# Performance work log

Hardware: AMD Instinct MI355X
Metric: run time of the kernel (lower is better)

The kernel has to match this reference:

```python
import jax, jax.numpy as jnp
import numpy as np

N_NODES = 100000
N_EDGES = 600000
IN_DIM = 128
HID = 128


def setup_inputs() -> dict:
    key = jax.random.key(0)
    ks = jax.random.split(key, 9)
    x = jax.random.normal(ks[0], (N_NODES, IN_DIM), dtype=jnp.float32)
    edge_index = jax.random.randint(ks[1], (2, N_EDGES), 0, N_NODES, dtype=jnp.int64)
    s = 1.0 / np.sqrt(IN_DIM)
    # PyG SAGEConv: out = lin_l(mean_aggr(x_src)) + lin_r(x_root); lin_l carries the bias.
    W_l0 = jax.random.uniform(ks[2], (IN_DIM, HID), jnp.float32, -s, s)
    b_l0 = jnp.zeros((HID,), jnp.float32)
    W_r0 = jax.random.uniform(ks[3], (IN_DIM, HID), jnp.float32, -s, s)
    s2 = 1.0 / np.sqrt(HID)
    W_l1 = jax.random.uniform(ks[4], (HID, HID), jnp.float32, -s2, s2)
    b_l1 = jnp.zeros((HID,), jnp.float32)
    W_r1 = jax.random.uniform(ks[5], (HID, HID), jnp.float32, -s2, s2)
    return {"x": x, "edge_index": edge_index,
            "W_l0": W_l0, "b_l0": b_l0, "W_r0": W_r0,
            "W_l1": W_l1, "b_l1": b_l1, "W_r1": W_r1}


def _sage_mean_conv(h, src, dst, W_l, b_l, W_r):
    # gather source-node features per edge, scatter-mean into destinations
    msgs = h[src]                                              # [E, D]
    sums = jax.ops.segment_sum(msgs, dst, num_segments=N_NODES)  # [N, D]
    cnt = jax.ops.segment_sum(jnp.ones((src.shape[0],), h.dtype), dst,
                              num_segments=N_NODES)             # [N]
    mean = sums / jnp.maximum(cnt, 1.0)[:, None]
    return mean @ W_l + b_l + h @ W_r


def reference(x, edge_index, W_l0, b_l0, W_r0, W_l1, b_l1, W_r1):
    src, dst = edge_index[0], edge_index[1]
    h = _sage_mean_conv(x, src, dst, W_l0, b_l0, W_r0)
    h = jax.nn.relu(h)  # dropout is identity in eval mode
    h = _sage_mean_conv(h, src, dst, W_l1, b_l1, W_r1)
    h = jax.nn.relu(h)
    return h
```

## Files before the change

### kernel.cpp

```cpp
#include <hip/hip_runtime.h>

#define N_NODES 100000
#define N_EDGES 600000
#define DIM 128

typedef __attribute__((ext_vector_type(8))) short bf16x8;
typedef __attribute__((ext_vector_type(4))) float f32x4;

typedef __attribute__((address_space(1))) const unsigned int g_u32;
typedef __attribute__((address_space(3))) unsigned int l_u32;
__device__ __forceinline__ void stage16(const void* g, void* l) {
  __builtin_amdgcn_global_load_lds((g_u32*)g, (l_u32*)l, 16, 0, 0);
}

__device__ __forceinline__ unsigned short f32_to_bf16_rn(float f) {
  unsigned int u = __builtin_bit_cast(unsigned int, f);
  unsigned int r = (u + 0x7FFFu + ((u >> 16) & 1u)) >> 16;
  return (unsigned short)r;
}

__global__ __launch_bounds__(256) void prep_k(
    const float* __restrict__ Wl0, const float* __restrict__ Wr0,
    const float* __restrict__ Wl1, const float* __restrict__ Wr1,
    unsigned short* __restrict__ P0, unsigned short* __restrict__ P1,
    const float* __restrict__ x, unsigned short* __restrict__ xhi,
    int* __restrict__ deg) {
  const int gid = blockIdx.x * 256 + threadIdx.x;
  if (gid < N_NODES) deg[gid] = 0;
  if (gid < 65536) {
    const int layer = gid >> 15;
    const int idx = gid & 32767;
    const int j = idx & 7;
    const int l = (idx >> 3) & 63;
    const int nt = (idx >> 9) & 7;
    const int g = idx >> 12;
    const int k = ((g & 3) << 5) + ((l >> 4) << 3) + j;
    const int n = (nt << 4) + (l & 15);
    const float* W = layer ? ((g < 4) ? Wl1 : Wr1) : ((g < 4) ? Wl0 : Wr0);
    (layer ? P1 : P0)[idx] = f32_to_bf16_rn(W[k * 128 + n]);
  } else {
    const int i = gid - 65536;
    if (i < N_NODES * DIM / 4) {
      const float4 v = reinterpret_cast<const float4*>(x)[i];
      const float f[4] = {v.x, v.y, v.z, v.w};
      unsigned short h[4];
#pragma unroll
      for (int j = 0; j < 4; ++j) h[j] = f32_to_bf16_rn(f[j]);
      uint2 hp;
      hp.x = (unsigned)h[0] | ((unsigned)h[1] << 16);
      hp.y = (unsigned)h[2] | ((unsigned)h[3] << 16);
      reinterpret_cast<uint2*>(xhi)[i] = hp;
    }
  }
}

__global__ void hist_k(const int* __restrict__ dst, int* __restrict__ deg) {
  int e = blockIdx.x * blockDim.x + threadIdx.x;
  if (e < N_EDGES) atomicAdd(&deg[dst[e]], 1);
}

__global__ __launch_bounds__(1024) void scan1_k(const int* __restrict__ deg,
                                                int* __restrict__ incl,
                                                int* __restrict__ bsum) {
  __shared__ int wsum[16];
  const int t = threadIdx.x, lane = t & 63, w = t >> 6;
  const int gi = blockIdx.x * 1024 + t;
  int v = (gi < N_NODES) ? deg[gi] : 0;
  int s = v;
#pragma unroll
  for (int off = 1; off < 64; off <<= 1) {
    int u = __shfl_up(s, off);
    if (lane >= off) s += u;
  }
  if (lane == 63) wsum[w] = s;
  __syncthreads();
  if (t < 16) {
    int ws = wsum[t];
#pragma unroll
    for (int off = 1; off < 16; off <<= 1) {
      int u = __shfl_up(ws, off);
      if (t >= off) ws += u;
    }
    wsum[t] = ws;
  }
  __syncthreads();
  const int val = s + (w ? wsum[w - 1] : 0);
  if (gi < N_NODES) incl[gi] = val;
  if (t == 1023) bsum[blockIdx.x] = val;
}

__global__ __launch_bounds__(1024) void scan3_k(const int* __restrict__ deg,
                                                const int* __restrict__ incl,
                                                const int* __restrict__ bsum,
                                                int* __restrict__ rowptr,
                                                int* __restrict__ head) {
  __shared__ int spart[2];
  __shared__ int boff_s;
  const int t = threadIdx.x;
  if (t < 128) {
    int v = (t < blockIdx.x) ? bsum[t] : 0;
#pragma unroll
    for (int off = 1; off < 64; off <<= 1) v += __shfl_xor(v, off);
    if ((t & 63) == 0) spart[t >> 6] = v;
  }
  __syncthreads();
  if (t == 0) boff_s = spart[0] + spart[1];
  __syncthreads();
  const int gi = blockIdx.x * 1024 + t;
  if (gi < N_NODES) {
    const int e = incl[gi] - deg[gi] + boff_s;
    rowptr[gi] = e;
    head[gi] = e;
  }
  if (gi == 0) rowptr[N_NODES] = N_EDGES;
}

__global__ void fill_k(const int* __restrict__ src, const int* __restrict__ dst,
                       int* __restrict__ head, int* __restrict__ col) {
  int e = blockIdx.x * blockDim.x + threadIdx.x;
  if (e < N_EDGES) {
    int p = atomicAdd(&head[dst[e]], 1);
    col[p] = src[e];
  }
}

__global__ __launch_bounds__(256) void agg_k(
    const unsigned short* __restrict__ plane, const int* __restrict__ rowptr,
    const int* __restrict__ col, unsigned short* __restrict__ mhi) {
  const int t = threadIdx.x;
  const int node = blockIdx.x * 16 + (t >> 4);
  const int q = t & 15;
  const int beg = rowptr[node], end = rowptr[node + 1];
  const uint4* P = reinterpret_cast<const uint4*>(plane);
  float a[8] = {};

  auto accum = [&](uint4 v) {
    const unsigned int u[4] = {v.x, v.y, v.z, v.w};
#pragma unroll
    for (int w = 0; w < 4; ++w) {
      a[2 * w] += __builtin_bit_cast(float, u[w] << 16);
      a[2 * w + 1] += __builtin_bit_cast(float, u[w] & 0xFFFF0000u);
    }
  };

  for (int i = beg; i < end; i += 4) {
    const int i1 = min(i + 1, end - 1);
    const int i2 = min(i + 2, end - 1);
    const int i3 = min(i + 3, end - 1);
    const int c0 = col[i], c1 = col[i1], c2 = col[i2], c3 = col[i3];
    const uint4 v0 = P[(size_t)c0 * 16 + q];
    const uint4 v1 = P[(size_t)c1 * 16 + q];
    const uint4 v2 = P[(size_t)c2 * 16 + q];
    const uint4 v3 = P[(size_t)c3 * 16 + q];
    accum(v0);
    if (i + 1 < end) accum(v1);
    if (i + 2 < end) accum(v2);
    if (i + 3 < end) accum(v3);
  }

  const int d = end - beg;
  const float inv = 1.0f / (float)(d > 1 ? d : 1);
  unsigned int hw[4];
#pragma unroll
  for (int w = 0; w < 4; ++w) {
    const unsigned short h0 = f32_to_bf16_rn(a[2 * w] * inv);
    const unsigned short h1 = f32_to_bf16_rn(a[2 * w + 1] * inv);
    hw[w] = (unsigned)h0 | ((unsigned)h1 << 16);
  }
  uint4 ho = {hw[0], hw[1], hw[2], hw[3]};
  reinterpret_cast<uint4*>(mhi)[(size_t)node * 16 + q] = ho;
}

template <int OUTF32>
__global__ __launch_bounds__(256, 4) void gemm_k(
    const unsigned short* __restrict__ Mhi, const unsigned short* __restrict__ Hhi,
    const unsigned short* __restrict__ Bp, const float* __restrict__ bias,
    unsigned short* __restrict__ Ohi, float* __restrict__ Of) {
  __shared__ unsigned short Bl[4][4096];
  const int t = threadIdx.x;
  const int lane = t & 63;
  const int wid = t >> 6;
  const int rbase = blockIdx.x * 64 + wid * 16;
  const int lm = lane & 15, lk = lane >> 4;
  const size_t r0 = (size_t)min(rbase + lm, N_NODES - 1);

  f32x4 acc[8] = {};

  auto stageG = [&](int g, int nb) {
#pragma unroll
    for (int c = 0; c < 2; ++c) {
      const int e = (c * 256 + t) * 8;
      stage16(Bp + (size_t)g * 4096 + e, &Bl[nb][e]);
    }
  };
  auto loadA = [&](int g) {
    const unsigned short* P = (g < 4) ? Mhi : Hhi;
    const int ke = ((g & 3) << 5) + (lk << 3);
    return *reinterpret_cast<const bf16x8*>(P + r0 * DIM + ke);
  };

  stageG(0, 0);
  stageG(1, 1);
  bf16x8 ca0 = loadA(0), ca1 = loadA(1), na0, na1;
  __syncthreads();

#pragma unroll
  for (int pg = 0; pg < 4; ++pg) {
    const int b0 = (2 * pg) & 3, b1 = (2 * pg + 1) & 3;
    if (pg < 3) {
      stageG(2 * pg + 2, (b0 + 2) & 3);
      stageG(2 * pg + 3, (b1 + 2) & 3);
      na0 = loadA(2 * pg + 2);
      na1 = loadA(2 * pg + 3);
    }
#pragma unroll
    for (int nt = 0; nt < 8; ++nt) {
      const bf16x8 b =
          *reinterpret_cast<const bf16x8*>(&Bl[b0][(nt * 64 + lane) * 8]);
      acc[nt] = __builtin_amdgcn_mfma_f32_16x16x32_bf16(ca0, b, acc[nt], 0, 0, 0);
    }
#pragma unroll
    for (int nt = 0; nt < 8; ++nt) {
      const bf16x8 b =
          *reinterpret_cast<const bf16x8*>(&Bl[b1][(nt * 64 + lane) * 8]);
      acc[nt] = __builtin_amdgcn_mfma_f32_16x16x32_bf16(ca1, b, acc[nt], 0, 0, 0);
    }
    __syncthreads();
    ca0 = na0;
    ca1 = na1;
  }

#pragma unroll
  for (int nt = 0; nt < 8; ++nt) {
    const int cidx = nt * 16 + lm;
    const float bv = bias[cidx];
#pragma unroll
    for (int i = 0; i < 4; ++i) {
      const int r = rbase + lk * 4 + i;
      if (r < N_NODES) {
        float v = acc[nt][i] + bv;
        v = fmaxf(v, 0.0f);
        if (OUTF32) {
          Of[(size_t)r * DIM + cidx] = v;
        } else {
          Ohi[(size_t)r * DIM + cidx] = f32_to_bf16_rn(v);
        }
      }
    }
  }
}

extern "C" void kernel_launch(void* const* d_in, const int* in_sizes, int n_in,
                              void* d_out, int out_size, void* d_ws,
                              size_t ws_size, hipStream_t stream) {
  const float* x = (const float*)d_in[0];
  const int* ei = (const int*)d_in[1];
  const float* Wl0 = (const float*)d_in[2];
  const float* bl0 = (const float*)d_in[3];
  const float* Wr0 = (const float*)d_in[4];
  const float* Wl1 = (const float*)d_in[5];
  const float* bl1 = (const float*)d_in[6];
  const float* Wr1 = (const float*)d_in[7];
  float* out = (float*)d_out;
  const int* src = ei;
  const int* dst = ei + N_EDGES;

  char* p = (char*)d_ws;
  auto alloc = [&](size_t bytes) {
    char* q = p;
    p += (bytes + 255) & ~(size_t)255;
    return q;
  };
  int* deg = (int*)alloc((size_t)N_NODES * 4);
  int* rowptr = (int*)alloc((size_t)(N_NODES + 1) * 4);
  int* head = (int*)alloc((size_t)N_NODES * 4);
  int* col = (int*)alloc((size_t)N_EDGES * 4);
  int* bsum = (int*)alloc(128 * 4);
  unsigned short* Bp0 = (unsigned short*)alloc(32768 * 2);
  unsigned short* Bp1 = (unsigned short*)alloc(32768 * 2);
  unsigned short* xhi = (unsigned short*)alloc((size_t)N_NODES * DIM * 2);
  unsigned short* mhi = (unsigned short*)alloc((size_t)N_NODES * DIM * 2);
  unsigned short* h1hi = (unsigned short*)alloc((size_t)N_NODES * DIM * 2);

  const int nScanB = (N_NODES + 1023) / 1024;

  prep_k<<<(65536 + N_NODES * DIM / 4 + 255) / 256, 256, 0, stream>>>(
      Wl0, Wr0, Wl1, Wr1, Bp0, Bp1, x, xhi, deg);
  hist_k<<<(N_EDGES + 255) / 256, 256, 0, stream>>>(dst, deg);
  scan1_k<<<nScanB, 1024, 0, stream>>>(deg, head, bsum);
  scan3_k<<<nScanB, 1024, 0, stream>>>(deg, head, bsum, rowptr, head);
  fill_k<<<(N_EDGES + 255) / 256, 256, 0, stream>>>(src, dst, head, col);

  const int nBlocks = (N_NODES + 63) / 64;
  const int aggBlocks = N_NODES / 16;

  agg_k<<<aggBlocks, 256, 0, stream>>>(xhi, rowptr, col, mhi);
  gemm_k<0><<<nBlocks, 256, 0, stream>>>(mhi, xhi, Bp0, bl0, h1hi, nullptr);
  agg_k<<<aggBlocks, 256, 0, stream>>>(h1hi, rowptr, col, mhi);
  gemm_k<1><<<nBlocks, 256, 0, stream>>>(mhi, h1hi, Bp1, bl1, nullptr, out);
}
```

Before: 182.0 us.

## Split GEMM tile by output columns per wave and drop block barriers

Each wave now covers all 64 rows of the block and a 32-column slice, instead of 16 rows and all 128 columns. Each wave therefore stages and reads only its own B fragments, which removes the block-wide __syncthreads. The LDS buffer shrinks to double buffering, and pipelining is done with explicit vmcnt waits. The trade-off is that A rows are now loaded redundantly by all four waves, four times more global or L2 reads of A, in exchange for less B LDS traffic and no barriers.

```diff
diff --git a/kernel.cpp b/kernel.cpp
--- a/kernel.cpp
+++ b/kernel.cpp
@@ -176,74 +176,85 @@
     const unsigned short* __restrict__ Mhi, const unsigned short* __restrict__ Hhi,
     const unsigned short* __restrict__ Bp, const float* __restrict__ bias,
     unsigned short* __restrict__ Ohi, float* __restrict__ Of) {
-  __shared__ unsigned short Bl[4][4096];
+  __shared__ unsigned short Bl[2][4096];
   const int t = threadIdx.x;
   const int lane = t & 63;
   const int wid = t >> 6;
-  const int rbase = blockIdx.x * 64 + wid * 16;
+  const int rbase = blockIdx.x * 64;
   const int lm = lane & 15, lk = lane >> 4;
-  const size_t r0 = (size_t)min(rbase + lm, N_NODES - 1);
-
-  f32x4 acc[8] = {};
+  size_t r[4];
+#pragma unroll
+  for (int mt = 0; mt < 4; ++mt)
+    r[mt] = (size_t)min(rbase + mt * 16 + lm, N_NODES - 1);
+
+  f32x4 acc[4][2] = {};
 
   auto stageG = [&](int g, int nb) {
 #pragma unroll
-    for (int c = 0; c < 2; ++c) {
-      const int e = (c * 256 + t) * 8;
-      stage16(Bp + (size_t)g * 4096 + e, &Bl[nb][e]);
+    for (int s = 0; s < 2; ++s) {
+      const int nt = 2 * wid + s;
+      stage16(Bp + ((size_t)(g * 8 + nt) * 64 + lane) * 8,
+              &Bl[nb][(nt * 64 + lane) * 8]);
     }
   };
-  auto loadA = [&](int g) {
+  auto loadA = [&](int g, bf16x8* a) {
     const unsigned short* P = (g < 4) ? Mhi : Hhi;
     const int ke = ((g & 3) << 5) + (lk << 3);
-    return *reinterpret_cast<const bf16x8*>(P + r0 * DIM + ke);
+#pragma unroll
+    for (int mt = 0; mt < 4; ++mt)
+      a[mt] = *reinterpret_cast<const bf16x8*>(P + r[mt] * DIM + ke);
   };
 
+  bf16x8 ca[4], na[4];
   stageG(0, 0);
-  stageG(1, 1);
-  bf16x8 ca0 = loadA(0), ca1 = loadA(1), na0, na1;
-  __syncthreads();
-
-#pragma unroll
-  for (int pg = 0; pg < 4; ++pg) {
-    const int b0 = (2 * pg) & 3, b1 = (2 * pg + 1) & 3;
-    if (pg < 3) {
-      stageG(2 * pg + 2, (b0 + 2) & 3);
-      stageG(2 * pg + 3, (b1 + 2) & 3);
-      na0 = loadA(2 * pg + 2);
-      na1 = loadA(2 * pg + 3);
-    }
-#pragma unroll
-    for (int nt = 0; nt < 8; ++nt) {
+  loadA(0, ca);
+
+#pragma unroll
+  for (int g = 0; g < 8; ++g) {
+    const int buf = g & 1;
+    if (g < 7) {
+      stageG(g + 1, buf ^ 1);
+      loadA(g + 1, na);
+      __builtin_amdgcn_sched_barrier(0);
+      asm volatile("s_waitcnt vmcnt(6)" ::: "memory");
+      __builtin_amdgcn_sched_barrier(0);
+    } else {
+      __builtin_amdgcn_sched_barrier(0);
+      asm volatile("s_waitcnt vmcnt(0)" ::: "memory");
+      __builtin_amdgcn_sched_barrier(0);
+    }
+#pragma unroll
+    for (int s = 0; s < 2; ++s) {
+      const int nt = 2 * wid + s;
       const bf16x8 b =
-          *reinterpret_cast<const bf16x8*>(&Bl[b0][(nt * 64 + lane) * 8]);
-      acc[nt] = __builtin_amdgcn_mfma_f32_16x16x32_bf16(ca0, b, acc[nt], 0, 0, 0);
-    }
-#pragma unroll
-    for (int nt = 0; nt < 8; ++nt) {
-      const bf16x8 b =
-          *reinterpret_cast<const bf16x8*>(&Bl[b1][(nt * 64 + lane) * 8]);
-      acc[nt] = __builtin_amdgcn_mfma_f32_16x16x32_bf16(ca1, b, acc[nt], 0, 0, 0);
-    }
-    __syncthreads();
-    ca0 = na0;
-    ca1 = na1;
-  }
-
-#pragma unroll
-  for (int nt = 0; nt < 8; ++nt) {
-    const int cidx = nt * 16 + lm;
+          *reinterpret_cast<const bf16x8*>(&Bl[buf][(nt * 64 + lane) * 8]);
+#pragma unroll
+      for (int mt = 0; mt < 4; ++mt)
+        acc[mt][s] = __builtin_amdgcn_mfma_f32_16x16x32_bf16(ca[mt], b, acc[mt][s], 0, 0, 0);
+    }
+    if (g < 7) {
+#pragma unroll
+      for (int mt = 0; mt < 4; ++mt) ca[mt] = na[mt];
+    }
+  }
+
+#pragma unroll
+  for (int s = 0; s < 2; ++s) {
+    const int cidx = (2 * wid + s) * 16 + lm;
     const float bv = bias[cidx];
 #pragma unroll
-    for (int i = 0; i < 4; ++i) {
-      const int r = rbase + lk * 4 + i;
-      if (r < N_NODES) {
-        float v = acc[nt][i] + bv;
-        v = fmaxf(v, 0.0f);
-        if (OUTF32) {
-          Of[(size_t)r * DIM + cidx] = v;
-        } else {
-          Ohi[(size_t)r * DIM + cidx] = f32_to_bf16_rn(v);
+    for (int mt = 0; mt < 4; ++mt) {
+#pragma unroll
+      for (int i = 0; i < 4; ++i) {
+        const int rr = rbase + mt * 16 + lk * 4 + i;
+        if (rr < N_NODES) {
+          float v = acc[mt][s][i] + bv;
+          v = fmaxf(v, 0.0f);
+          if (OUTF32) {
+            Of[(size_t)rr * DIM + cidx] = v;
+          } else {
+            Ohi[(size_t)rr * DIM + cidx] = f32_to_bf16_rn(v);
+          }
         }
       }
     }
```

New measurement: 214.0 us. 1.18x slower.

## Reorder layer-2 as transform-then-aggregate and fuse both GEMMs into one kernel

Applied to the files above, without the earlier changes.

Since mean aggregation is linear, layer 2 now computes P = h1·W_l1 and Q = h1·W_r1 + b right after the layer-1 GEMM, keeping h1 in swizzled LDS so it never goes to global memory. The final aggregation gathers rows of P, averages them, adds Q and applies ReLU, writing fp32 output directly. This removes one GEMM launch, the round trip of h1 and mhi through memory, and one pass over the aggregation intermediate. In exchange it writes two bf16 planes (P and Q) instead of one, and P is rounded to bf16 before averaging, which slightly changes the numerics.

```diff
diff --git a/kernel.cpp b/kernel.cpp
--- a/kernel.cpp
+++ b/kernel.cpp
@@ -17,6 +17,12 @@
   unsigned int u = __builtin_bit_cast(unsigned int, f);
   unsigned int r = (u + 0x7FFFu + ((u >> 16) & 1u)) >> 16;
   return (unsigned short)r;
+}
+__device__ __forceinline__ float bf16lo(unsigned int u) {
+  return __builtin_bit_cast(float, u << 16);
+}
+__device__ __forceinline__ float bf16hi(unsigned int u) {
+  return __builtin_bit_cast(float, u & 0xFFFF0000u);
 }
 
 __global__ __launch_bounds__(256) void prep_k(
@@ -138,8 +144,8 @@
     const unsigned int u[4] = {v.x, v.y, v.z, v.w};
 #pragma unroll
     for (int w = 0; w < 4; ++w) {
-      a[2 * w] += __builtin_bit_cast(float, u[w] << 16);
-      a[2 * w + 1] += __builtin_bit_cast(float, u[w] & 0xFFFF0000u);
+      a[2 * w] += bf16lo(u[w]);
+      a[2 * w + 1] += bf16hi(u[w]);
     }
   };
 
@@ -171,12 +177,13 @@
   reinterpret_cast<uint4*>(mhi)[(size_t)node * 16 + q] = ho;
 }
 
-template <int OUTF32>
-__global__ __launch_bounds__(256, 4) void gemm_k(
-    const unsigned short* __restrict__ Mhi, const unsigned short* __restrict__ Hhi,
-    const unsigned short* __restrict__ Bp, const float* __restrict__ bias,
-    unsigned short* __restrict__ Ohi, float* __restrict__ Of) {
-  __shared__ unsigned short Bl[4][4096];
+__global__ __launch_bounds__(256, 4) void gemm01_k(
+    const unsigned short* __restrict__ Mhi, const unsigned short* __restrict__ Xhi,
+    const unsigned short* __restrict__ Bp0, const float* __restrict__ bl0,
+    const unsigned short* __restrict__ Bp1, const float* __restrict__ bl1,
+    unsigned short* __restrict__ P1, unsigned short* __restrict__ Q1) {
+  __shared__ unsigned short Bl[2][4096];
+  __shared__ unsigned short H1t[4][2048];
   const int t = threadIdx.x;
   const int lane = t & 63;
   const int wid = t >> 6;
@@ -184,70 +191,152 @@
   const int lm = lane & 15, lk = lane >> 4;
   const size_t r0 = (size_t)min(rbase + lm, N_NODES - 1);
 
-  f32x4 acc[8] = {};
-
-  auto stageG = [&](int g, int nb) {
+  auto stageG = [&](const unsigned short* Bp, int g, int nb) {
 #pragma unroll
     for (int c = 0; c < 2; ++c) {
       const int e = (c * 256 + t) * 8;
       stage16(Bp + (size_t)g * 4096 + e, &Bl[nb][e]);
     }
   };
+
+  f32x4 acc[8] = {};
   auto loadA = [&](int g) {
-    const unsigned short* P = (g < 4) ? Mhi : Hhi;
+    const unsigned short* P = (g < 4) ? Mhi : Xhi;
     const int ke = ((g & 3) << 5) + (lk << 3);
     return *reinterpret_cast<const bf16x8*>(P + r0 * DIM + ke);
   };
-
-  stageG(0, 0);
-  stageG(1, 1);
-  bf16x8 ca0 = loadA(0), ca1 = loadA(1), na0, na1;
-  __syncthreads();
-
-#pragma unroll
-  for (int pg = 0; pg < 4; ++pg) {
-    const int b0 = (2 * pg) & 3, b1 = (2 * pg + 1) & 3;
-    if (pg < 3) {
-      stageG(2 * pg + 2, (b0 + 2) & 3);
-      stageG(2 * pg + 3, (b1 + 2) & 3);
-      na0 = loadA(2 * pg + 2);
-      na1 = loadA(2 * pg + 3);
+  stageG(Bp0, 0, 0);
+  bf16x8 ca = loadA(0), na;
+  __syncthreads();
+#pragma unroll
+  for (int g = 0; g < 8; ++g) {
+    const int buf = g & 1;
+    if (g < 7) {
+      stageG(Bp0, g + 1, buf ^ 1);
+      na = loadA(g + 1);
     }
 #pragma unroll
     for (int nt = 0; nt < 8; ++nt) {
       const bf16x8 b =
-          *reinterpret_cast<const bf16x8*>(&Bl[b0][(nt * 64 + lane) * 8]);
-      acc[nt] = __builtin_amdgcn_mfma_f32_16x16x32_bf16(ca0, b, acc[nt], 0, 0, 0);
+          *reinterpret_cast<const bf16x8*>(&Bl[buf][(nt * 64 + lane) * 8]);
+      acc[nt] = __builtin_amdgcn_mfma_f32_16x16x32_bf16(ca, b, acc[nt], 0, 0, 0);
+    }
+    __syncthreads();
+    ca = na;
+  }
+
+  unsigned short* ht = H1t[wid];
+#pragma unroll
+  for (int nt = 0; nt < 8; ++nt) {
+    const int c2 = nt * 16 + lm;
+    const float bv = bl0[c2];
+#pragma unroll
+    for (int i = 0; i < 4; ++i) {
+      const int row = lk * 4 + i;
+      const float v = fmaxf(acc[nt][i] + bv, 0.0f);
+      const int byte = (row << 8) + (c2 << 1);
+      const int sw = byte ^ ((row & 7) << 4);
+      *reinterpret_cast<unsigned short*>(reinterpret_cast<char*>(ht) + sw) =
+          f32_to_bf16_rn(v);
+    }
+  }
+
+  f32x4 accP[8] = {}, accQ[8] = {};
+  auto loadH = [&](int g) {
+    const int byte = (lm << 8) + ((((g & 3) << 5) + (lk << 3)) << 1);
+    const int sw = byte ^ ((lm & 7) << 4);
+    return *reinterpret_cast<const bf16x8*>(
+        reinterpret_cast<const char*>(ht) + sw);
+  };
+  stageG(Bp1, 0, 0);
+  bf16x8 ha = loadH(0), hn;
+  __syncthreads();
+#pragma unroll
+  for (int g = 0; g < 8; ++g) {
+    const int buf = g & 1;
+    if (g < 7) {
+      stageG(Bp1, g + 1, buf ^ 1);
+      hn = loadH(g + 1);
     }
 #pragma unroll
     for (int nt = 0; nt < 8; ++nt) {
       const bf16x8 b =
-          *reinterpret_cast<const bf16x8*>(&Bl[b1][(nt * 64 + lane) * 8]);
-      acc[nt] = __builtin_amdgcn_mfma_f32_16x16x32_bf16(ca1, b, acc[nt], 0, 0, 0);
+          *reinterpret_cast<const bf16x8*>(&Bl[buf][(nt * 64 + lane) * 8]);
+      if (g < 4) {
+        accP[nt] = __builtin_amdgcn_mfma_f32_16x16x32_bf16(ha, b, accP[nt], 0, 0, 0);
+      } else {
+        accQ[nt] = __builtin_amdgcn_mfma_f32_16x16x32_bf16(ha, b, accQ[nt], 0, 0, 0);
+      }
     }
     __syncthreads();
-    ca0 = na0;
-    ca1 = na1;
+    ha = hn;
   }
 
 #pragma unroll
   for (int nt = 0; nt < 8; ++nt) {
     const int cidx = nt * 16 + lm;
-    const float bv = bias[cidx];
+    const float bq = bl1[cidx];
 #pragma unroll
     for (int i = 0; i < 4; ++i) {
       const int r = rbase + lk * 4 + i;
       if (r < N_NODES) {
-        float v = acc[nt][i] + bv;
-        v = fmaxf(v, 0.0f);
-        if (OUTF32) {
-          Of[(size_t)r * DIM + cidx] = v;
-        } else {
-          Ohi[(size_t)r * DIM + cidx] = f32_to_bf16_rn(v);
-        }
+        P1[(size_t)r * DIM + cidx] = f32_to_bf16_rn(accP[nt][i]);
+        Q1[(size_t)r * DIM + cidx] = f32_to_bf16_rn(accQ[nt][i] + bq);
       }
     }
   }
+}
+
+__global__ __launch_bounds__(256) void agg1f_k(
+    const unsigned short* __restrict__ P1, const unsigned short* __restrict__ Q1,
+    const int* __restrict__ rowptr, const int* __restrict__ col,
+    float* __restrict__ out) {
+  const int t = threadIdx.x;
+  const int node = blockIdx.x * 16 + (t >> 4);
+  const int q = t & 15;
+  const int beg = rowptr[node], end = rowptr[node + 1];
+  const uint4* P = reinterpret_cast<const uint4*>(P1);
+  float a[8] = {};
+
+  auto accum = [&](uint4 v) {
+    const unsigned int u[4] = {v.x, v.y, v.z, v.w};
+#pragma unroll
+    for (int w = 0; w < 4; ++w) {
+      a[2 * w] += bf16lo(u[w]);
+      a[2 * w + 1] += bf16hi(u[w]);
+    }
+  };
+
+  for (int i = beg; i < end; i += 4) {
+    const int i1 = min(i + 1, end - 1);
+    const int i2 = min(i + 2, end - 1);
+    const int i3 = min(i + 3, end - 1);
+    const int c0 = col[i], c1 = col[i1], c2 = col[i2], c3 = col[i3];
+    const uint4 v0 = P[(size_t)c0 * 16 + q];
+    const uint4 v1 = P[(size_t)c1 * 16 + q];
+    const uint4 v2 = P[(size_t)c2 * 16 + q];
+    const uint4 v3 = P[(size_t)c3 * 16 + q];
+    accum(v0);
+    if (i + 1 < end) accum(v1);
+    if (i + 2 < end) accum(v2);
+    if (i + 3 < end) accum(v3);
+  }
+
+  const int d = end - beg;
+  const float inv = 1.0f / (float)(d > 1 ? d : 1);
+  const uint4 qv = reinterpret_cast<const uint4*>(Q1)[(size_t)node * 16 + q];
+  const unsigned int qu[4] = {qv.x, qv.y, qv.z, qv.w};
+  float o[8];
+#pragma unroll
+  for (int w = 0; w < 4; ++w) {
+    o[2 * w] = fmaxf(a[2 * w] * inv + bf16lo(qu[w]), 0.0f);
+    o[2 * w + 1] = fmaxf(a[2 * w + 1] * inv + bf16hi(qu[w]), 0.0f);
+  }
+  float4 o0 = {o[0], o[1], o[2], o[3]};
+  float4 o1 = {o[4], o[5], o[6], o[7]};
+  float4* op = reinterpret_cast<float4*>(out + (size_t)node * DIM + q * 8);
+  op[0] = o0;
+  op[1] = o1;
 }
 
 extern "C" void kernel_launch(void* const* d_in, const int* in_sizes, int n_in,
@@ -280,7 +369,8 @@
   unsigned short* Bp1 = (unsigned short*)alloc(32768 * 2);
   unsigned short* xhi = (unsigned short*)alloc((size_t)N_NODES * DIM * 2);
   unsigned short* mhi = (unsigned short*)alloc((size_t)N_NODES * DIM * 2);
-  unsigned short* h1hi = (unsigned short*)alloc((size_t)N_NODES * DIM * 2);
+  unsigned short* P1hi = (unsigned short*)alloc((size_t)N_NODES * DIM * 2);
+  unsigned short* Q1hi = (unsigned short*)alloc((size_t)N_NODES * DIM * 2);
 
   const int nScanB = (N_NODES + 1023) / 1024;
 
@@ -295,7 +385,7 @@
   const int aggBlocks = N_NODES / 16;
 
   agg_k<<<aggBlocks, 256, 0, stream>>>(xhi, rowptr, col, mhi);
-  gemm_k<0><<<nBlocks, 256, 0, stream>>>(mhi, xhi, Bp0, bl0, h1hi, nullptr);
-  agg_k<<<aggBlocks, 256, 0, stream>>>(h1hi, rowptr, col, mhi);
-  gemm_k<1><<<nBlocks, 256, 0, stream>>>(mhi, h1hi, Bp1, bl1, nullptr, out);
-}
+  gemm01_k<<<nBlocks, 256, 0, stream>>>(mhi, xhi, Bp0, bl0, Bp1, bl1, P1hi,
+                                        Q1hi);
+  agg1f_k<<<aggBlocks, 256, 0, stream>>>(P1hi, Q1hi, rowptr, col, out);
+}
```

After: 179.3 us. Within noise of the previous version (-1.5%).

## Halve GEMM LDS to two buffers and stage bf16 output through LDS

Applied to the files above, without the earlier changes.

The GEMM k-loop goes from four LDS buffers, two k-groups per step, to two buffers with one k-group per step, which halves shared memory per block and may raise occupancy. In the bf16-output layer, results are first written to LDS and then copied out as coalesced 16-byte row stores, instead of scattered 2-byte global stores. The cost is more barriers per block, less prefetch depth in the k-loop, and an extra LDS round trip in the epilogue.

```diff
diff --git a/kernel.cpp b/kernel.cpp
--- a/kernel.cpp
+++ b/kernel.cpp
@@ -17,6 +17,12 @@
   unsigned int u = __builtin_bit_cast(unsigned int, f);
   unsigned int r = (u + 0x7FFFu + ((u >> 16) & 1u)) >> 16;
   return (unsigned short)r;
+}
+__device__ __forceinline__ float bf16lo(unsigned int u) {
+  return __builtin_bit_cast(float, u << 16);
+}
+__device__ __forceinline__ float bf16hi(unsigned int u) {
+  return __builtin_bit_cast(float, u & 0xFFFF0000u);
 }
 
 __global__ __launch_bounds__(256) void prep_k(
@@ -138,8 +144,8 @@
     const unsigned int u[4] = {v.x, v.y, v.z, v.w};
 #pragma unroll
     for (int w = 0; w < 4; ++w) {
-      a[2 * w] += __builtin_bit_cast(float, u[w] << 16);
-      a[2 * w + 1] += __builtin_bit_cast(float, u[w] & 0xFFFF0000u);
+      a[2 * w] += bf16lo(u[w]);
+      a[2 * w + 1] += bf16hi(u[w]);
     }
   };
 
@@ -176,7 +182,7 @@
     const unsigned short* __restrict__ Mhi, const unsigned short* __restrict__ Hhi,
     const unsigned short* __restrict__ Bp, const float* __restrict__ bias,
     unsigned short* __restrict__ Ohi, float* __restrict__ Of) {
-  __shared__ unsigned short Bl[4][4096];
+  __shared__ unsigned short Bl[2][4096];
   const int t = threadIdx.x;
   const int lane = t & 63;
   const int wid = t >> 6;
@@ -200,52 +206,61 @@
   };
 
   stageG(0, 0);
-  stageG(1, 1);
-  bf16x8 ca0 = loadA(0), ca1 = loadA(1), na0, na1;
-  __syncthreads();
-
-#pragma unroll
-  for (int pg = 0; pg < 4; ++pg) {
-    const int b0 = (2 * pg) & 3, b1 = (2 * pg + 1) & 3;
-    if (pg < 3) {
-      stageG(2 * pg + 2, (b0 + 2) & 3);
-      stageG(2 * pg + 3, (b1 + 2) & 3);
-      na0 = loadA(2 * pg + 2);
-      na1 = loadA(2 * pg + 3);
+  bf16x8 ca = loadA(0), na;
+  __syncthreads();
+
+#pragma unroll
+  for (int g = 0; g < 8; ++g) {
+    const int buf = g & 1;
+    if (g < 7) {
+      stageG(g + 1, buf ^ 1);
+      na = loadA(g + 1);
     }
 #pragma unroll
     for (int nt = 0; nt < 8; ++nt) {
       const bf16x8 b =
-          *reinterpret_cast<const bf16x8*>(&Bl[b0][(nt * 64 + lane) * 8]);
-      acc[nt] = __builtin_amdgcn_mfma_f32_16x16x32_bf16(ca0, b, acc[nt], 0, 0, 0);
-    }
+          *reinterpret_cast<const bf16x8*>(&Bl[buf][(nt * 64 + lane) * 8]);
+      acc[nt] = __builtin_amdgcn_mfma_f32_16x16x32_bf16(ca, b, acc[nt], 0, 0, 0);
+    }
+    __syncthreads();
+    ca = na;
+  }
+
+  if (OUTF32) {
 #pragma unroll
     for (int nt = 0; nt < 8; ++nt) {
-      const bf16x8 b =
-          *reinterpret_cast<const bf16x8*>(&Bl[b1][(nt * 64 + lane) * 8]);
-      acc[nt] = __builtin_amdgcn_mfma_f32_16x16x32_bf16(ca1, b, acc[nt], 0, 0, 0);
+      const int cidx = nt * 16 + lm;
+      const float bv = bias[cidx];
+#pragma unroll
+      for (int i = 0; i < 4; ++i) {
+        const int r = rbase + lk * 4 + i;
+        if (r < N_NODES)
+          Of[(size_t)r * DIM + cidx] = fmaxf(acc[nt][i] + bv, 0.0f);
+      }
+    }
+  } else {
+    unsigned short* flat = &Bl[0][0];
+    unsigned short* wt = flat + wid * 2048;
+#pragma unroll
+    for (int nt = 0; nt < 8; ++nt) {
+      const int cidx = nt * 16 + lm;
+      const float bv = bias[cidx];
+#pragma unroll
+      for (int i = 0; i < 4; ++i) {
+        const int row = lk * 4 + i;
+        wt[row * 128 + cidx] = f32_to_bf16_rn(fmaxf(acc[nt][i] + bv, 0.0f));
+      }
     }
     __syncthreads();
-    ca0 = na0;
-    ca1 = na1;
-  }
-
-#pragma unroll
-  for (int nt = 0; nt < 8; ++nt) {
-    const int cidx = nt * 16 + lm;
-    const float bv = bias[cidx];
-#pragma unroll
-    for (int i = 0; i < 4; ++i) {
-      const int r = rbase + lk * 4 + i;
-      if (r < N_NODES) {
-        float v = acc[nt][i] + bv;
-        v = fmaxf(v, 0.0f);
-        if (OUTF32) {
-          Of[(size_t)r * DIM + cidx] = v;
-        } else {
-          Ohi[(size_t)r * DIM + cidx] = f32_to_bf16_rn(v);
-        }
-      }
+    const int row = t >> 2;
+    const int seg = t & 3;
+    const int gr = blockIdx.x * 64 + row;
+    if (gr < N_NODES) {
+      const uint4* sp =
+          reinterpret_cast<const uint4*>(flat + row * 128 + seg * 32);
+      uint4* dp = reinterpret_cast<uint4*>(Ohi + (size_t)gr * DIM + seg * 32);
+#pragma unroll
+      for (int k = 0; k < 4; ++k) dp[k] = sp[k];
     }
   }
 }
```

Result: faster. 177.3 us (-2.5%).
